# Performance work log

Measured on AMD Instinct MI355X. Metric: run time of the kernel, lower is better.

The kernel has to match this reference:

```python
import jax, jax.numpy as jnp
import numpy as np


def dequantize_sparse_sinq(W_q, scales, zeros, mask, scale2, group_size):
    """SINQ-style dual-scaled grouped dequant with sparsity mask.

    W = ((W_q - zeros) * scales) broadcast over groups along the in-dim,
    then scaled per input column by scale2, then masked (pruned weights -> 0).
    W_q: [O, I] int; scales/zeros: [O, I//g]; scale2: [I]; mask: [O, I] bool.
    """
    O, I = W_q.shape
    g = group_size
    Wq = W_q.astype(jnp.float32).reshape(O, I // g, g)
    W = (Wq - zeros[:, :, None]) * scales[:, :, None]  # grouped affine dequant
    W = W.reshape(O, I) * scale2[None, :]              # second (column) scale
    return jnp.where(mask, W, jnp.zeros((), dtype=W.dtype))


def setup_inputs() -> dict:
    key = jax.random.key(0)
    ks = jax.random.split(key, 7)
    B, S, I, O, G = 8, 2048, 4096, 4096, 128
    x = jax.random.normal(ks[0], (B, S, I), dtype=jnp.float32)
    W_q = jax.random.randint(ks[1], (O, I), 0, 16, dtype=jnp.int32)
    scales = jax.random.uniform(ks[2], (O, I // G), dtype=jnp.float32)
    zeros = jax.random.uniform(ks[3], (O, I // G), dtype=jnp.float32)
    mask = jax.random.randint(ks[4], (O, I), 0, 2, dtype=jnp.int32).astype(jnp.bool_)
    scale2 = jax.random.uniform(ks[5], (I,), dtype=jnp.float32)
    bias = jax.random.normal(ks[6], (O,), dtype=jnp.float32)
    return {"x": x, "W_q": W_q, "scales": scales, "zeros": zeros,
            "mask": mask, "scale2": scale2, "bias": bias, "group_size": G}


def reference(x, W_q, scales, zeros, mask, scale2, bias, group_size):
    W = dequantize_sparse_sinq(W_q, scales, zeros, mask, scale2, group_size)
    W = W.astype(x.dtype)
    out = jnp.einsum('bsi,oi->bso', x, W)  # matmul(x, W.T)
    out = out + bias
    return out
```

## Files before the change

kernel.cpp:

```cpp
#include <hip/hip_runtime.h>
#include <hip/hip_bf16.h>
#include <stdint.h>


typedef short s16x8 __attribute__((ext_vector_type(8)));
typedef short s16x4 __attribute__((ext_vector_type(4)));
typedef float f32x4 __attribute__((ext_vector_type(4)));

#define BM 128
#define BN 128
#define BK 64
#define LDSS 72

static __device__ __forceinline__ short f2bf(float f) {
    __hip_bfloat16 h = __float2bfloat16(f);
    return *reinterpret_cast<short*>(&h);
}

__global__ __launch_bounds__(256)
void dequant_kernel(const int* __restrict__ Wq,
                    const float* __restrict__ scales,
                    const float* __restrict__ zeros,
                    const void* __restrict__ mask_raw,
                    const float* __restrict__ scale2,
                    short* __restrict__ Wb,
                    int O, int I, int G) {
    __shared__ int lds_flag;
    if (threadIdx.x == 0) lds_flag = 0;
    __syncthreads();
    {
        unsigned v = ((const unsigned*)mask_raw)[threadIdx.x & 255];
        if (v > 1u) lds_flag = 1;
    }
    __syncthreads();
    const bool mask_is_byte = (lds_flag != 0);

    int idx = (blockIdx.x * 256 + threadIdx.x) * 8;
    if (idx >= O * I) return;
    int o = idx / I;
    int i = idx - o * I;
    int gi = o * (I / G) + i / G;
    float s = scales[gi];
    float z = zeros[gi];

    int4 w0 = *(const int4*)(Wq + idx);
    int4 w1 = *(const int4*)(Wq + idx + 4);
    float4 s2a = *(const float4*)(scale2 + i);
    float4 s2b = *(const float4*)(scale2 + i + 4);

    unsigned m[8];
    if (mask_is_byte) {
        unsigned long long mb = *(const unsigned long long*)((const unsigned char*)mask_raw + idx);
        #pragma unroll
        for (int j = 0; j < 8; ++j) m[j] = (unsigned)((mb >> (8 * j)) & 0xffULL);
    } else {
        int4 ma = *(const int4*)((const int*)mask_raw + idx);
        int4 mbv = *(const int4*)((const int*)mask_raw + idx + 4);
        m[0] = ma.x;  m[1] = ma.y;  m[2] = ma.z;  m[3] = ma.w;
        m[4] = mbv.x; m[5] = mbv.y; m[6] = mbv.z; m[7] = mbv.w;
    }

    float v[8];
    v[0] = ((float)w0.x - z) * s * s2a.x;
    v[1] = ((float)w0.y - z) * s * s2a.y;
    v[2] = ((float)w0.z - z) * s * s2a.z;
    v[3] = ((float)w0.w - z) * s * s2a.w;
    v[4] = ((float)w1.x - z) * s * s2b.x;
    v[5] = ((float)w1.y - z) * s * s2b.y;
    v[6] = ((float)w1.z - z) * s * s2b.z;
    v[7] = ((float)w1.w - z) * s * s2b.w;

    union { s16x8 v; int4 q; } out;
    #pragma unroll
    for (int j = 0; j < 8; ++j) {
        float masked = m[j] ? v[j] : 0.0f;
        out.v[j] = f2bf(masked);
    }
    *(int4*)(Wb + idx) = out.q;
}

__global__ __launch_bounds__(256)
void convert_x_kernel(const float* __restrict__ X, short* __restrict__ Xb, int n8) {
    int c = blockIdx.x * 256 + threadIdx.x;
    if (c >= n8) return;
    size_t idx = (size_t)c * 8;
    float4 a = *(const float4*)(X + idx);
    float4 b = *(const float4*)(X + idx + 4);
    union { s16x8 v; int4 q; } o;
    o.v[0] = f2bf(a.x); o.v[1] = f2bf(a.y); o.v[2] = f2bf(a.z); o.v[3] = f2bf(a.w);
    o.v[4] = f2bf(b.x); o.v[5] = f2bf(b.y); o.v[6] = f2bf(b.z); o.v[7] = f2bf(b.w);
    *(int4*)(Xb + idx) = o.q;
}

__global__ __launch_bounds__(256, 2)
void gemm_bb_kernel(const short* __restrict__ Xb,
                    const short* __restrict__ Wb,
                    const float* __restrict__ bias,
                    float* __restrict__ Out,
                    int M, int N, int K) {
    __shared__ short As[BM * BK];
    __shared__ short Bs[BN * BK];

    const int tid  = threadIdx.x;
    const int m0   = blockIdx.y * BM;
    const int n0   = blockIdx.x * BN;
    const int wave = tid >> 6;
    const int lane = tid & 63;
    const int wm   = (wave >> 1) * 64;
    const int wn   = (wave & 1) * 64;
    const int lr   = lane & 15;
    const int lq   = lane >> 4;

    f32x4 acc[4][4] = {};

    const short* gA = Xb + (size_t)(m0 + (tid >> 3)) * K + (tid & 7) * 8;
    const short* gB = Wb + (size_t)(n0 + (tid >> 3)) * K + (tid & 7) * 8;
    short* lA = &As[wave * 512];
    short* lB = &Bs[wave * 512];

    for (int k0 = 0; k0 < K; k0 += BK) {
        #pragma unroll
        for (int t = 0; t < 4; ++t) {
            __builtin_amdgcn_global_load_lds(
                (const __attribute__((address_space(1))) void*)(gA + (size_t)t * 32 * K + k0),
                (__attribute__((address_space(3))) void*)(lA + t * 2048), 16, 0, 0);
            __builtin_amdgcn_global_load_lds(
                (const __attribute__((address_space(1))) void*)(gB + (size_t)t * 32 * K + k0),
                (__attribute__((address_space(3))) void*)(lB + t * 2048), 16, 0, 0);
        }
        __syncthreads();

        #pragma unroll
        for (int kk = 0; kk < BK; kk += 32) {
            s16x8 af[4], bfv[4];
            #pragma unroll
            for (int mi = 0; mi < 4; ++mi)
                af[mi] = *(const s16x8*)&As[(wm + mi * 16 + lr) * BK + kk + lq * 8];
            #pragma unroll
            for (int ni = 0; ni < 4; ++ni)
                bfv[ni] = *(const s16x8*)&Bs[(wn + ni * 16 + lr) * BK + kk + lq * 8];
            #pragma unroll
            for (int mi = 0; mi < 4; ++mi)
                #pragma unroll
                for (int ni = 0; ni < 4; ++ni)
                    acc[mi][ni] = __builtin_amdgcn_mfma_f32_16x16x32_bf16(
                        af[mi], bfv[ni], acc[mi][ni], 0, 0, 0);
        }
        __syncthreads();
    }

    #pragma unroll
    for (int ni = 0; ni < 4; ++ni) {
        int nc = n0 + wn + ni * 16 + lr;
        float bv = bias[nc];
        #pragma unroll
        for (int mi = 0; mi < 4; ++mi) {
            int mr = m0 + wm + mi * 16 + lq * 4;
            #pragma unroll
            for (int r = 0; r < 4; ++r)
                Out[(size_t)(mr + r) * N + nc] = acc[mi][ni][r] + bv;
        }
    }
}

__global__ __launch_bounds__(256, 2)
void gemm_kernel(const float* __restrict__ X,
                 const short* __restrict__ Wb,
                 const float* __restrict__ bias,
                 float* __restrict__ Out,
                 int M, int N, int K) {
    __shared__ short As[BM * LDSS];
    __shared__ short Bs[BN * LDSS];

    const int tid  = threadIdx.x;
    const int m0   = blockIdx.y * BM;
    const int n0   = blockIdx.x * BN;
    const int wave = tid >> 6;
    const int lane = tid & 63;
    const int wm   = (wave >> 1) * 64;
    const int wn   = (wave & 1) * 64;
    const int lr   = lane & 15;
    const int lq   = lane >> 4;

    f32x4 acc[4][4] = {};

    for (int k0 = 0; k0 < K; k0 += BK) {
        #pragma unroll
        for (int t = 0; t < 8; ++t) {
            int c   = tid + t * 256;
            int row = c >> 4;
            int col = (c & 15) * 4;
            float4 xv = *(const float4*)(X + (size_t)(m0 + row) * K + k0 + col);
            s16x4 bv;
            bv[0] = f2bf(xv.x); bv[1] = f2bf(xv.y);
            bv[2] = f2bf(xv.z); bv[3] = f2bf(xv.w);
            *(s16x4*)&As[row * LDSS + col] = bv;
        }
        #pragma unroll
        for (int t = 0; t < 4; ++t) {
            int c   = tid + t * 256;
            int row = c >> 3;
            int col = (c & 7) * 8;
            s16x8 wv = *(const s16x8*)(Wb + (size_t)(n0 + row) * K + k0 + col);
            *(s16x8*)&Bs[row * LDSS + col] = wv;
        }
        __syncthreads();

        #pragma unroll
        for (int kk = 0; kk < BK; kk += 32) {
            s16x8 af[4], bf[4];
            #pragma unroll
            for (int mi = 0; mi < 4; ++mi)
                af[mi] = *(const s16x8*)&As[(wm + mi * 16 + lr) * LDSS + kk + lq * 8];
            #pragma unroll
            for (int ni = 0; ni < 4; ++ni)
                bf[ni] = *(const s16x8*)&Bs[(wn + ni * 16 + lr) * LDSS + kk + lq * 8];
            #pragma unroll
            for (int mi = 0; mi < 4; ++mi)
                #pragma unroll
                for (int ni = 0; ni < 4; ++ni)
                    acc[mi][ni] = __builtin_amdgcn_mfma_f32_16x16x32_bf16(
                        af[mi], bf[ni], acc[mi][ni], 0, 0, 0);
        }
        __syncthreads();
    }

    #pragma unroll
    for (int ni = 0; ni < 4; ++ni) {
        int nc = n0 + wn + ni * 16 + lr;
        float bv = bias[nc];
        #pragma unroll
        for (int mi = 0; mi < 4; ++mi) {
            int mr = m0 + wm + mi * 16 + lq * 4;
            #pragma unroll
            for (int r = 0; r < 4; ++r)
                Out[(size_t)(mr + r) * N + nc] = acc[mi][ni][r] + bv;
        }
    }
}

extern "C" void kernel_launch(void* const* d_in, const int* in_sizes, int n_in,
                              void* d_out, int out_size, void* d_ws, size_t ws_size,
                              hipStream_t stream) {
    const float* x      = (const float*)d_in[0];
    const int*   Wq     = (const int*)d_in[1];
    const float* scales = (const float*)d_in[2];
    const float* zeros  = (const float*)d_in[3];
    const void*  mask   = (const void*)d_in[4];
    const float* scale2 = (const float*)d_in[5];
    const float* bias   = (const float*)d_in[6];
    float*       out    = (float*)d_out;

    const int I = in_sizes[5];
    const int O = in_sizes[6];
    const int M = (int)(in_sizes[0] / I);
    const int G = (int)(((long long)O * I) / in_sizes[2]);

    short* Wb = (short*)d_ws;
    size_t wbBytes = (size_t)O * I * sizeof(short);
    size_t xbBytes = (size_t)M * I * sizeof(short);

    long long totalW = (long long)O * I;
    int dq_blocks = (int)((totalW / 8 + 255) / 256);
    dequant_kernel<<<dq_blocks, 256, 0, stream>>>(Wq, scales, zeros, mask,
                                                  scale2, Wb, O, I, G);

    dim3 grid(O / BN, M / BM);
    if (ws_size >= wbBytes + xbBytes) {
        short* Xb = (short*)((char*)d_ws + wbBytes);
        int n8 = (int)(((size_t)M * I) / 8);
        int cv_blocks = (n8 + 255) / 256;
        convert_x_kernel<<<cv_blocks, 256, 0, stream>>>(x, Xb, n8);
        gemm_bb_kernel<<<grid, 256, 0, stream>>>(Xb, Wb, bias, out, M, O, I);
    } else {
        gemm_kernel<<<grid, 256, 0, stream>>>(x, Wb, bias, out, M, O, I);
    }
}
```

Measured before the change: 1.142 ms.

## Replace bf16 GEMM with 256x256 8-wave pipelined kernel using swizzled LDS

Replaces the 128x128 single-buffered bf16 GEMM with a 256x256 tile, 512-thread kernel. It uses a 4-stage LDS ring fed by global_load_lds with explicit vmcnt waits, and XOR-swizzled LDS addressing to avoid bank conflicts. It also adds XCD-aware block remapping and s_setprio around the MFMA bursts. The aim is to hide global-load latency behind MFMA work and raise arithmetic intensity per tile, at the cost of more LDS (128KB per block) and more register pressure from 32 accumulators per lane.

```diff
diff --git a/kernel.cpp b/kernel.cpp
--- a/kernel.cpp
+++ b/kernel.cpp
@@ -7,10 +7,9 @@
 typedef short s16x4 __attribute__((ext_vector_type(4)));
 typedef float f32x4 __attribute__((ext_vector_type(4)));
 
-#define BM 128
-#define BN 128
-#define BK 64
-#define LDSS 72
+#define BM 256
+#define BN 256
+#define BK 32
 
 static __device__ __forceinline__ short f2bf(float f) {
     __hip_bfloat16 h = __float2bfloat16(f);
@@ -92,18 +91,150 @@
     *(int4*)(Xb + idx) = o.q;
 }
 
+__global__ __launch_bounds__(512, 2)
+void gemm8_kernel(const short* __restrict__ Xb,
+                  const short* __restrict__ Wb,
+                  const float* __restrict__ bias,
+                  float* __restrict__ Out,
+                  int M, int N, int K) {
+    __shared__ short lds[4 * 16384];
+
+    const int tid  = threadIdx.x;
+    const int wave = tid >> 6;
+    const int lane = tid & 63;
+    const int lr   = lane & 15;
+    const int lq   = lane >> 4;
+    const int sw   = (lr >> 1) & 3;
+    const int wm   = (wave >> 2) * 128;
+    const int wn   = (wave & 3) * 64;
+
+    const int gx  = gridDim.x;
+    const int nwg = gx * gridDim.y;
+    int bid = blockIdx.y * gx + blockIdx.x;
+    if ((nwg & 7) == 0) {
+        int cpx = nwg >> 3;
+        bid = (bid & 7) * cpx + (bid >> 3);
+    }
+    const int bx = bid % gx;
+    const int by = bid / gx;
+    const int m0 = by * BM;
+    const int n0 = bx * BN;
+
+    const int NT = K / BK;
+
+    const int srow = tid >> 2;
+    const int scol = (((tid & 3) ^ ((tid >> 3) & 3))) * 8;
+    const short* gA = Xb + (size_t)(m0 + srow) * K + scol;
+    const short* gB = Wb + (size_t)(n0 + srow) * K + scol;
+
+    const int laneA = (wm + lr) * 32 + ((lq ^ sw) << 3);
+    const int laneB = 8192 + (wn + lr) * 32 + ((lq ^ sw) << 3);
+    const int dstA = wave * 512;
+    const int dstB = 8192 + wave * 512;
+
+    f32x4 acc[8][4] = {};
+
+    #define STAGE_A(t_) do {                                                    \
+        int b_  = ((t_) & 3) * 16384;                                           \
+        int k_  = (t_) * BK;                                                    \
+        __builtin_amdgcn_global_load_lds(                                       \
+            (const __attribute__((address_space(1))) void*)(gA + (size_t)k_),   \
+            (__attribute__((address_space(3))) void*)(lds + b_ + dstA), 16, 0, 0); \
+        __builtin_amdgcn_global_load_lds(                                       \
+            (const __attribute__((address_space(1))) void*)(gA + (size_t)128 * K + k_), \
+            (__attribute__((address_space(3))) void*)(lds + b_ + dstA + 4096), 16, 0, 0); \
+    } while (0)
+    #define STAGE_B(t_) do {                                                    \
+        int b_  = ((t_) & 3) * 16384;                                           \
+        int k_  = (t_) * BK;                                                    \
+        __builtin_amdgcn_global_load_lds(                                       \
+            (const __attribute__((address_space(1))) void*)(gB + (size_t)k_),   \
+            (__attribute__((address_space(3))) void*)(lds + b_ + dstB), 16, 0, 0); \
+        __builtin_amdgcn_global_load_lds(                                       \
+            (const __attribute__((address_space(1))) void*)(gB + (size_t)128 * K + k_), \
+            (__attribute__((address_space(3))) void*)(lds + b_ + dstB + 4096), 16, 0, 0); \
+    } while (0)
+
+    STAGE_A(0); STAGE_B(0);
+    STAGE_A(1); STAGE_B(1);
+    STAGE_A(2); STAGE_B(2);
+    asm volatile("s_waitcnt vmcnt(8)" ::: "memory");
+    __builtin_amdgcn_s_barrier();
+
+    for (int t = 0; t < NT; ++t) {
+        const short* base = lds + ((t & 3) << 14);
+        s16x8 bfr[4], af[4];
+
+        #pragma unroll
+        for (int ni = 0; ni < 4; ++ni)
+            bfr[ni] = *(const s16x8*)(base + laneB + ni * 512);
+        #pragma unroll
+        for (int mi = 0; mi < 4; ++mi)
+            af[mi] = *(const s16x8*)(base + laneA + mi * 512);
+        if (t < NT - 3) STAGE_A(t + 3);
+        __builtin_amdgcn_s_barrier();
+        __builtin_amdgcn_s_setprio(1);
+        #pragma unroll
+        for (int mi = 0; mi < 4; ++mi)
+            #pragma unroll
+            for (int ni = 0; ni < 4; ++ni)
+                acc[mi][ni] = __builtin_amdgcn_mfma_f32_16x16x32_bf16(
+                    af[mi], bfr[ni], acc[mi][ni], 0, 0, 0);
+        __builtin_amdgcn_s_setprio(0);
+        __builtin_amdgcn_s_barrier();
+
+        #pragma unroll
+        for (int mi = 0; mi < 4; ++mi)
+            af[mi] = *(const s16x8*)(base + laneA + (mi + 4) * 512);
+        if (t < NT - 3) STAGE_B(t + 3);
+        __builtin_amdgcn_s_barrier();
+        __builtin_amdgcn_s_setprio(1);
+        #pragma unroll
+        for (int mi = 0; mi < 4; ++mi)
+            #pragma unroll
+            for (int ni = 0; ni < 4; ++ni)
+                acc[mi + 4][ni] = __builtin_amdgcn_mfma_f32_16x16x32_bf16(
+                    af[mi], bfr[ni], acc[mi + 4][ni], 0, 0, 0);
+        __builtin_amdgcn_s_setprio(0);
+        if (t < NT - 3)       asm volatile("s_waitcnt vmcnt(8)" ::: "memory");
+        else if (t == NT - 3) asm volatile("s_waitcnt vmcnt(4)" ::: "memory");
+        else                  asm volatile("s_waitcnt vmcnt(0)" ::: "memory");
+        __builtin_amdgcn_s_barrier();
+    }
+    #undef STAGE_A
+    #undef STAGE_B
+
+    #pragma unroll
+    for (int ni = 0; ni < 4; ++ni) {
+        int nc = n0 + wn + ni * 16 + lr;
+        float bv = bias[nc];
+        #pragma unroll
+        for (int mi = 0; mi < 8; ++mi) {
+            int mr = m0 + wm + mi * 16 + lq * 4;
+            #pragma unroll
+            for (int r = 0; r < 4; ++r)
+                Out[(size_t)(mr + r) * N + nc] = acc[mi][ni][r] + bv;
+        }
+    }
+}
+
+#define FBM 128
+#define FBN 128
+#define FBK 64
+#define LDSS 72
+
 __global__ __launch_bounds__(256, 2)
-void gemm_bb_kernel(const short* __restrict__ Xb,
-                    const short* __restrict__ Wb,
-                    const float* __restrict__ bias,
-                    float* __restrict__ Out,
-                    int M, int N, int K) {
-    __shared__ short As[BM * BK];
-    __shared__ short Bs[BN * BK];
+void gemm_kernel(const float* __restrict__ X,
+                 const short* __restrict__ Wb,
+                 const float* __restrict__ bias,
+                 float* __restrict__ Out,
+                 int M, int N, int K) {
+    __shared__ short As[FBM * LDSS];
+    __shared__ short Bs[FBN * LDSS];
 
     const int tid  = threadIdx.x;
-    const int m0   = blockIdx.y * BM;
-    const int n0   = blockIdx.x * BN;
+    const int m0   = blockIdx.y * FBM;
+    const int n0   = blockIdx.x * FBN;
     const int wave = tid >> 6;
     const int lane = tid & 63;
     const int wm   = (wave >> 1) * 64;
@@ -113,78 +244,7 @@
 
     f32x4 acc[4][4] = {};
 
-    const short* gA = Xb + (size_t)(m0 + (tid >> 3)) * K + (tid & 7) * 8;
-    const short* gB = Wb + (size_t)(n0 + (tid >> 3)) * K + (tid & 7) * 8;
-    short* lA = &As[wave * 512];
-    short* lB = &Bs[wave * 512];
-
-    for (int k0 = 0; k0 < K; k0 += BK) {
-        #pragma unroll
-        for (int t = 0; t < 4; ++t) {
-            __builtin_amdgcn_global_load_lds(
-                (const __attribute__((address_space(1))) void*)(gA + (size_t)t * 32 * K + k0),
-                (__attribute__((address_space(3))) void*)(lA + t * 2048), 16, 0, 0);
-            __builtin_amdgcn_global_load_lds(
-                (const __attribute__((address_space(1))) void*)(gB + (size_t)t * 32 * K + k0),
-                (__attribute__((address_space(3))) void*)(lB + t * 2048), 16, 0, 0);
-        }
-        __syncthreads();
-
-        #pragma unroll
-        for (int kk = 0; kk < BK; kk += 32) {
-            s16x8 af[4], bfv[4];
-            #pragma unroll
-            for (int mi = 0; mi < 4; ++mi)
-                af[mi] = *(const s16x8*)&As[(wm + mi * 16 + lr) * BK + kk + lq * 8];
-            #pragma unroll
-            for (int ni = 0; ni < 4; ++ni)
-                bfv[ni] = *(const s16x8*)&Bs[(wn + ni * 16 + lr) * BK + kk + lq * 8];
-            #pragma unroll
-            for (int mi = 0; mi < 4; ++mi)
-                #pragma unroll
-                for (int ni = 0; ni < 4; ++ni)
-                    acc[mi][ni] = __builtin_amdgcn_mfma_f32_16x16x32_bf16(
-                        af[mi], bfv[ni], acc[mi][ni], 0, 0, 0);
-        }
-        __syncthreads();
-    }
-
-    #pragma unroll
-    for (int ni = 0; ni < 4; ++ni) {
-        int nc = n0 + wn + ni * 16 + lr;
-        float bv = bias[nc];
-        #pragma unroll
-        for (int mi = 0; mi < 4; ++mi) {
-            int mr = m0 + wm + mi * 16 + lq * 4;
-            #pragma unroll
-            for (int r = 0; r < 4; ++r)
-                Out[(size_t)(mr + r) * N + nc] = acc[mi][ni][r] + bv;
-        }
-    }
-}
-
-__global__ __launch_bounds__(256, 2)
-void gemm_kernel(const float* __restrict__ X,
-                 const short* __restrict__ Wb,
-                 const float* __restrict__ bias,
-                 float* __restrict__ Out,
-                 int M, int N, int K) {
-    __shared__ short As[BM * LDSS];
-    __shared__ short Bs[BN * LDSS];
-
-    const int tid  = threadIdx.x;
-    const int m0   = blockIdx.y * BM;
-    const int n0   = blockIdx.x * BN;
-    const int wave = tid >> 6;
-    const int lane = tid & 63;
-    const int wm   = (wave >> 1) * 64;
-    const int wn   = (wave & 1) * 64;
-    const int lr   = lane & 15;
-    const int lq   = lane >> 4;
-
-    f32x4 acc[4][4] = {};
-
-    for (int k0 = 0; k0 < K; k0 += BK) {
+    for (int k0 = 0; k0 < K; k0 += FBK) {
         #pragma unroll
         for (int t = 0; t < 8; ++t) {
             int c   = tid + t * 256;
@@ -207,7 +267,7 @@
         __syncthreads();
 
         #pragma unroll
-        for (int kk = 0; kk < BK; kk += 32) {
+        for (int kk = 0; kk < FBK; kk += 32) {
             s16x8 af[4], bf[4];
             #pragma unroll
             for (int mi = 0; mi < 4; ++mi)
@@ -265,14 +325,17 @@
     dequant_kernel<<<dq_blocks, 256, 0, stream>>>(Wq, scales, zeros, mask,
                                                   scale2, Wb, O, I, G);
 
-    dim3 grid(O / BN, M / BM);
-    if (ws_size >= wbBytes + xbBytes) {
+    const bool shape_ok = (M % BM == 0) && (O % BN == 0) && (I % BK == 0)
+                          && (I / BK >= 4);
+    if (shape_ok && ws_size >= wbBytes + xbBytes) {
         short* Xb = (short*)((char*)d_ws + wbBytes);
         int n8 = (int)(((size_t)M * I) / 8);
         int cv_blocks = (n8 + 255) / 256;
         convert_x_kernel<<<cv_blocks, 256, 0, stream>>>(x, Xb, n8);
-        gemm_bb_kernel<<<grid, 256, 0, stream>>>(Xb, Wb, bias, out, M, O, I);
+        dim3 grid(O / BN, M / BM);
+        gemm8_kernel<<<grid, 512, 0, stream>>>(Xb, Wb, bias, out, M, O, I);
     } else {
+        dim3 grid(O / FBN, M / FBM);
         gemm_kernel<<<grid, 256, 0, stream>>>(x, Wb, bias, out, M, O, I);
     }
 }
```

After: 994.7 us. 12.9% less time.
